# Performance work log

Measured on AMD Instinct MI355X. Metric: run time of the kernel, lower is better.

Reference implementation:

```python
import jax, jax.numpy as jnp
import numpy as np

B, N, E, A, H, F, HEADS = 2, 16384, 262144, 3, 128, 16, 4
DH = H // HEADS
CONST = (2.0 * np.pi) ** 0.5


def setup_inputs() -> dict:
    key = jax.random.key(0)
    ks = jax.random.split(key, 16)
    s = 0.05
    return {
        "x": jax.random.normal(ks[0], (B, N, H), jnp.float32),
        "edge_index": jax.random.randint(ks[1], (2, E), 0, N),
        # per-action message MLPs (self.mlp)
        "mlp_W1": jax.random.normal(ks[2], (A, H, H), jnp.float32) * s,
        "mlp_b1": jnp.zeros((A, H), jnp.float32),
        "mlp_W2": jax.random.normal(ks[3], (A, H, H), jnp.float32) * s,
        "mlp_b2": jnp.zeros((A, H), jnp.float32),
        # transformer (MMTs) projections, 4 heads over the action axis
        "Wq": jax.random.normal(ks[4], (H, H), jnp.float32) * s,
        "bq": jnp.zeros((H,), jnp.float32),
        "Wk": jax.random.normal(ks[5], (H, H), jnp.float32) * s,
        "bk": jnp.zeros((H,), jnp.float32),
        "Wv": jax.random.normal(ks[6], (H, H), jnp.float32) * s,
        "bv": jnp.zeros((H,), jnp.float32),
        "Wo": jax.random.normal(ks[7], (H, H), jnp.float32) * s,
        "bo": jnp.zeros((H,), jnp.float32),
        # decide_mu MLPs (decide_In_sigma is never used in the original forward)
        "mu_W1": jax.random.normal(ks[8], (A, H, H), jnp.float32) * s,
        "mu_b1": jnp.zeros((A, H), jnp.float32),
        "mu_W2": jax.random.normal(ks[9], (A, H, F), jnp.float32) * s,
        "mu_b2": jnp.zeros((A, F), jnp.float32),
    }


def _forward(x, edge_index, mlp_W1, mlp_b1, mlp_W2, mlp_b2,
             Wq, bq, Wk, bk, Wv, bv, Wo, bo, mu_W1, mu_b1, mu_W2, mu_b2):
    # per-action MLP stack: (B,N,H) -> (B,N,A,H)
    h = jax.nn.relu(jnp.einsum('bnh,ahk->bnak', x, mlp_W1) + mlp_b1)
    h = jnp.einsum('bnak,akh->bnah', h, mlp_W2) + mlp_b2
    # gather along source nodes, scatter-add into destination bins
    dst, src = edge_index[0], edge_index[1]
    g = h[:, src]                                   # (B,E,A,H) ~ 800 MB
    agg = jax.ops.segment_sum(jnp.moveaxis(g, 1, 0), dst, num_segments=N)
    agg = jnp.moveaxis(agg, 0, 1)                   # (B,N,A,H)
    # multi-head self-attention over the action axis (len A) per node
    q = (jnp.einsum('bnah,hk->bnak', agg, Wq) + bq).reshape(B, N, A, HEADS, DH)
    k = (jnp.einsum('bnah,hk->bnak', agg, Wk) + bk).reshape(B, N, A, HEADS, DH)
    v = (jnp.einsum('bnah,hk->bnak', agg, Wv) + bv).reshape(B, N, A, HEADS, DH)
    scores = jnp.einsum('bnqed,bnked->bneqk', q, k) / (DH ** 0.5)
    attn = jax.nn.softmax(scores, axis=-1)
    o = jnp.einsum('bneqk,bnked->bnqed', attn, v).reshape(B, N, A, H)
    h_I = agg + jnp.einsum('bnah,hk->bnak', o, Wo) + bo  # residual
    # per-action decode to action means: (B,N,A,F)
    m = jax.nn.relu(jnp.einsum('bnah,ahk->bnak', h_I, mu_W1) + mu_b1)
    mu = jnp.einsum('bnak,akf->bnaf', m, mu_W2) + mu_b2
    # Gaussian reparameterized sampling, VAR is a non-trainable all-ones buffer
    VAR = jnp.ones((N, A, F), jnp.float32)
    noise = jax.random.normal(jax.random.key(42), mu.shape, mu.dtype)
    sample = mu + noise * VAR
    logp = -jnp.log(CONST * VAR) - (sample - mu) ** 2 / (2.0 * VAR ** 2)
    a0 = jax.nn.softmax(jnp.tanh(sample[:, :, 0, :]), axis=-1)
    a1 = jax.nn.sigmoid(sample[:, :, 1, :])
    a2 = jnp.tanh(sample[:, :, 2, :])
    sample_out = jnp.stack([a0, a1, a2], axis=2)    # (B,N,A,F)
    return sample_out, logp.sum((-1, -2))           # ((B,N,A,F),(B,N))


def reference(x, edge_index, mlp_W1, mlp_b1, mlp_W2, mlp_b2,
              Wq, bq, Wk, bk, Wv, bv, Wo, bo, mu_W1, mu_b1, mu_W2, mu_b2):
    return _forward(x, edge_index, mlp_W1, mlp_b1, mlp_W2, mlp_b2,
                    Wq, bq, Wk, bk, Wv, bv, Wo, bo, mu_W1, mu_b1, mu_W2, mu_b2)
```

## Files before the change

### kernel.cpp

```cpp
#include <hip/hip_runtime.h>

#define NN    16384
#define EE    262144
#define BNODES 32768
#define AH    384
#define TOT_NOISE 1572864u

typedef __attribute__((ext_vector_type(8))) short short8;
typedef __attribute__((ext_vector_type(4))) float v4f;

__device__ __forceinline__ unsigned short f2bf(float f) {
  unsigned u = __float_as_uint(f);
  unsigned r = u + 0x7fffu + ((u >> 16) & 1u);
  return (unsigned short)(r >> 16);
}
__device__ __forceinline__ float bf2f(unsigned short h) {
  return __uint_as_float(((unsigned)h) << 16);
}
__device__ __forceinline__ float bflo(unsigned u) { return __uint_as_float(u << 16); }
__device__ __forceinline__ float bfhi(unsigned u) { return __uint_as_float(u & 0xffff0000u); }

__device__ __forceinline__ void threefry2x32_042(unsigned& x0, unsigned& x1) {
  const unsigned ks0 = 0u;
  const unsigned ks1 = 42u;
  const unsigned ks2 = 0x1BD11BDAu ^ 0u ^ 42u;
  x0 += ks0; x1 += ks1;
#define TFR(r) { x0 += x1; x1 = (x1 << (r)) | (x1 >> (32 - (r))); x1 ^= x0; }
  TFR(13) TFR(15) TFR(26) TFR(6)   x0 += ks1; x1 += ks2 + 1u;
  TFR(17) TFR(29) TFR(16) TFR(24)  x0 += ks2; x1 += ks0 + 2u;
  TFR(13) TFR(15) TFR(26) TFR(6)   x0 += ks0; x1 += ks1 + 3u;
  TFR(17) TFR(29) TFR(16) TFR(24)  x0 += ks1; x1 += ks2 + 4u;
  TFR(13) TFR(15) TFR(26) TFR(6)   x0 += ks2; x1 += ks0 + 5u;
#undef TFR
}

__device__ __forceinline__ float erfinv_f32(float x) {
  float w = -log1pf(-x * x);
  float p;
  if (w < 5.0f) {
    w -= 2.5f;
    p = 2.81022636e-08f;
    p = fmaf(p, w, 3.43273939e-07f);
    p = fmaf(p, w, -3.5233877e-06f);
    p = fmaf(p, w, -4.39150654e-06f);
    p = fmaf(p, w, 0.00021858087f);
    p = fmaf(p, w, -0.00125372503f);
    p = fmaf(p, w, -0.00417768164f);
    p = fmaf(p, w, 0.246640727f);
    p = fmaf(p, w, 1.50140941f);
  } else {
    w = sqrtf(w) - 3.0f;
    p = -0.000200214257f;
    p = fmaf(p, w, 0.000100950558f);
    p = fmaf(p, w, 0.00134934322f);
    p = fmaf(p, w, -0.00367342844f);
    p = fmaf(p, w, 0.00573950773f);
    p = fmaf(p, w, -0.0076224613f);
    p = fmaf(p, w, 0.00943887047f);
    p = fmaf(p, w, 1.00167406f);
    p = fmaf(p, w, 2.83297682f);
  }
  return p * x;
}

__device__ __forceinline__ unsigned jax_random_bits32(unsigned i) {
  unsigned x0 = 0u, x1 = i;
  threefry2x32_042(x0, x1);
  return x0 ^ x1;
}

__device__ __forceinline__ float jax_normal_from_bits(unsigned bits) {
  float f = __uint_as_float((bits >> 9) | 0x3f800000u) - 1.0f;
  const float lo = -0.99999994f;
  float u = f * 2.0f + lo;
  u = fmaxf(u, lo);
  return 1.4142135623730951f * erfinv_f32(u);
}

__global__ void edge_count(const int* __restrict__ dst, int* __restrict__ deg) {
  int e = blockIdx.x * 256 + threadIdx.x;
  if (e < EE) atomicAdd(&deg[dst[e]], 1);
}

__global__ __launch_bounds__(256) void scan_k(const int* __restrict__ deg,
                                              int* __restrict__ offs,
                                              int* __restrict__ cur) {
  __shared__ int part[256];
  int t = threadIdx.x;
  int base = t * 64;
  int s = 0;
  for (int i = 0; i < 64; i++) s += deg[base + i];
  part[t] = s;
  __syncthreads();
  for (int off = 1; off < 256; off <<= 1) {
    int v = (t >= off) ? part[t - off] : 0;
    __syncthreads();
    part[t] += v;
    __syncthreads();
  }
  int run = (t == 0) ? 0 : part[t - 1];
  for (int i = 0; i < 64; i++) {
    offs[base + i] = run;
    cur[base + i] = run;
    run += deg[base + i];
  }
  if (t == 255) offs[NN] = run;
}

__global__ void edge_fill(const int* __restrict__ dst, const int* __restrict__ srcv,
                          int* __restrict__ cur, int* __restrict__ csr) {
  int e = blockIdx.x * 256 + threadIdx.x;
  if (e < EE) {
    int d = dst[e];
    int p = atomicAdd(&cur[d], 1);
    csr[p] = srcv[e];
  }
}

__global__ __launch_bounds__(256) void prep_wfrag(
    const float* __restrict__ W1, const float* __restrict__ W2,
    const float* __restrict__ mW1,
    const float* __restrict__ Wq, const float* __restrict__ Wk,
    const float* __restrict__ Wv, const float* __restrict__ Wo,
    unsigned short* __restrict__ F) {
  int m = blockIdx.y;
  const float* W;
  if (m < 3) W = W1 + (long)m * 16384;
  else if (m < 6) W = W2 + (long)(m - 3) * 16384;
  else if (m < 9) W = mW1 + (long)(m - 6) * 16384;
  else W = (m == 9) ? Wq : (m == 10) ? Wk : (m == 11) ? Wv : Wo;
  int f = blockIdx.x * 256 + threadIdx.x;
  int tile = f >> 9;
  int kt = tile >> 3, nt = tile & 7;
  int r = f & 511;
  int lane = r >> 3, j = r & 7;
  int k = kt * 32 + (lane >> 4) * 8 + j;
  int n = nt * 16 + (lane & 15);
  F[(long)m * 16384 + f] = f2bf(W[k * 128 + n]);
}

__global__ __launch_bounds__(256) void prep_w2frag(
    const float* __restrict__ mW2, unsigned short* __restrict__ F2) {
  int a = blockIdx.y;
  int f = blockIdx.x * 256 + threadIdx.x;
  int kt = f >> 9;
  int r = f & 511;
  int lane = r >> 3, j = r & 7;
  int k = kt * 32 + (lane >> 4) * 8 + j;
  int n = lane & 15;
  F2[a * 2048 + f] = f2bf(mW2[(a * 128 + k) * 16 + n]);
}

#define GXSTR 136
__global__ __launch_bounds__(256, 4) void mlp_fused(
    const float* __restrict__ X,
    const unsigned short* __restrict__ WF1, const float* __restrict__ b1,
    const unsigned short* __restrict__ WF2, const float* __restrict__ b2,
    unsigned short* __restrict__ H) {
  __shared__ __align__(16) unsigned short As[128 * GXSTR];
  const int a = blockIdx.y;
  const long m0 = (long)blockIdx.x * 128;
  const int tid = threadIdx.x;
  const unsigned short* Wp1 = WF1 + (long)a * 16384;
  const unsigned short* Wp2 = WF2 + (long)a * 16384;

#pragma unroll
  for (int p = 0; p < 8; p++) {
    int c = tid + p * 256;
    int row = c >> 4, c8 = (c & 15) * 8;
    float4 v1 = *(const float4*)(X + (m0 + row) * 128 + c8);
    float4 v2 = *(const float4*)(X + (m0 + row) * 128 + c8 + 4);
    short8 o;
    o[0] = (short)f2bf(v1.x); o[1] = (short)f2bf(v1.y);
    o[2] = (short)f2bf(v1.z); o[3] = (short)f2bf(v1.w);
    o[4] = (short)f2bf(v2.x); o[5] = (short)f2bf(v2.y);
    o[6] = (short)f2bf(v2.z); o[7] = (short)f2bf(v2.w);
    *(short8*)(&As[row * GXSTR + c8]) = o;
  }
  __syncthreads();

  const int w = tid >> 6, l = tid & 63, lr = l & 15, lg = l >> 4;

  v4f acc[8][2];
#pragma unroll
  for (int mt = 0; mt < 8; mt++) {
    acc[mt][0] = (v4f){0.f, 0.f, 0.f, 0.f};
    acc[mt][1] = (v4f){0.f, 0.f, 0.f, 0.f};
  }
#pragma unroll
  for (int kt = 0; kt < 4; kt++) {
    short8 bfr[2];
#pragma unroll
    for (int ntl = 0; ntl < 2; ntl++)
      bfr[ntl] = *(const short8*)(Wp1 + (long)(kt * 8 + 2 * w + ntl) * 512 + l * 8);
#pragma unroll
    for (int mt = 0; mt < 8; mt++) {
      short8 af = *(const short8*)(&As[(mt * 16 + lr) * GXSTR + kt * 32 + lg * 8]);
      acc[mt][0] = __builtin_amdgcn_mfma_f32_16x16x32_bf16(af, bfr[0], acc[mt][0], 0, 0, 0);
      acc[mt][1] = __builtin_amdgcn_mfma_f32_16x16x32_bf16(af, bfr[1], acc[mt][1], 0, 0, 0);
    }
  }
  __syncthreads();

  {
    float bv[2] = {b1[a * 128 + 32 * w + lr], b1[a * 128 + 32 * w + 16 + lr]};
#pragma unroll
    for (int mt = 0; mt < 8; mt++)
#pragma unroll
      for (int ntl = 0; ntl < 2; ntl++)
#pragma unroll
        for (int i = 0; i < 4; i++) {
          int row = mt * 16 + lg * 4 + i;
          int col = 32 * w + ntl * 16 + lr;
          As[row * GXSTR + col] = f2bf(fmaxf(acc[mt][ntl][i] + bv[ntl], 0.0f));
        }
  }
  __syncthreads();

#pragma unroll
  for (int mt = 0; mt < 8; mt++) {
    acc[mt][0] = (v4f){0.f, 0.f, 0.f, 0.f};
    acc[mt][1] = (v4f){0.f, 0.f, 0.f, 0.f};
  }
#pragma unroll
  for (int kt = 0; kt < 4; kt++) {
    short8 bfr[2];
#pragma unroll
    for (int ntl = 0; ntl < 2; ntl++)
      bfr[ntl] = *(const short8*)(Wp2 + (long)(kt * 8 + 2 * w + ntl) * 512 + l * 8);
#pragma unroll
    for (int mt = 0; mt < 8; mt++) {
      short8 af = *(const short8*)(&As[(mt * 16 + lr) * GXSTR + kt * 32 + lg * 8]);
      acc[mt][0] = __builtin_amdgcn_mfma_f32_16x16x32_bf16(af, bfr[0], acc[mt][0], 0, 0, 0);
      acc[mt][1] = __builtin_amdgcn_mfma_f32_16x16x32_bf16(af, bfr[1], acc[mt][1], 0, 0, 0);
    }
  }
  {
    float bv[2] = {b2[a * 128 + 32 * w + lr], b2[a * 128 + 32 * w + 16 + lr]};
#pragma unroll
    for (int mt = 0; mt < 8; mt++)
#pragma unroll
      for (int ntl = 0; ntl < 2; ntl++)
#pragma unroll
        for (int i = 0; i < 4; i++) {
          long row = m0 + mt * 16 + lg * 4 + i;
          int col = 32 * w + ntl * 16 + lr;
          H[row * 384 + a * 128 + col] = f2bf(acc[mt][ntl][i] + bv[ntl]);
        }
  }
}

__global__ __launch_bounds__(192) void aggregate_v3(
    const unsigned short* __restrict__ H, const int* __restrict__ offs,
    const int* __restrict__ csr, unsigned short* __restrict__ AGB) {
  const int bid = blockIdx.x;
  const int bt = bid >> 13;
  const int pair = bid & 8191;
  const int t = threadIdx.x;
  const int n = pair * 2 + (t / 96);
  const int c = (t % 96) * 4;
  const int e0 = offs[n], e1 = offs[n + 1];
  const unsigned short* hb = H + (long)bt * NN * 384 + c;
  float a0 = 0.f, a1 = 0.f, a2 = 0.f, a3 = 0.f;

  const int nfull = (e1 - e0) >> 3;
  int s[8];
  if (nfull > 0) {
#pragma unroll
    for (int i = 0; i < 8; i++) s[i] = csr[e0 + i];
  }
  for (int b = 0; b < nfull; b++) {
    int sn[8];
    if (b + 1 < nfull) {
      int base = e0 + b * 8 + 8;
#pragma unroll
      for (int i = 0; i < 8; i++) sn[i] = csr[base + i];
    }
#pragma unroll
    for (int i = 0; i < 8; i++) {
      uint2 u = *(const uint2*)(hb + (long)s[i] * 384);
      a0 += bflo(u.x); a1 += bfhi(u.x); a2 += bflo(u.y); a3 += bfhi(u.y);
    }
#pragma unroll
    for (int i = 0; i < 8; i++) s[i] = sn[i];
  }
  for (int j = e0 + nfull * 8; j < e1; j++) {
    int si = csr[j];
    uint2 u = *(const uint2*)(hb + (long)si * 384);
    a0 += bflo(u.x); a1 += bfhi(u.x); a2 += bflo(u.y); a3 += bfhi(u.y);
  }
  uint2 out;
  out.x = (unsigned)f2bf(a0) | ((unsigned)f2bf(a1) << 16);
  out.y = (unsigned)f2bf(a2) | ((unsigned)f2bf(a3) << 16);
  *(uint2*)(AGB + ((long)bt * NN + n) * 384 + c) = out;
}

#define XSTR 136
#define QSTR 34
__global__ __launch_bounds__(256, 3) void attn_mega(
    const unsigned short* __restrict__ AGB, const unsigned short* __restrict__ WF,
    const float* __restrict__ bq, const float* __restrict__ bk,
    const float* __restrict__ bv, const float* __restrict__ bo,
    const unsigned short* __restrict__ WM1, const float* __restrict__ mb1,
    const unsigned short* __restrict__ WM2, const float* __restrict__ mb2,
    float* __restrict__ out0, float* __restrict__ out1) {
  __shared__ __align__(16) unsigned short xS[48 * XSTR];
  __shared__ __align__(16) unsigned short qS[4 * 48 * QSTR];
  __shared__ __align__(16) unsigned short kS[4 * 48 * QSTR];
  __shared__ __align__(16) unsigned short vS[4 * 48 * QSTR];
  __shared__ float lpS[48];

  const int tid = threadIdx.x;
  const long node0 = (long)blockIdx.x * 16;
  const unsigned short* src = AGB + node0 * 384;

#pragma unroll
  for (int p = 0; p < 3; p++) {
    int c = tid + p * 256;
    int row = c >> 4, c8 = (c & 15) * 8;
    short8 v = *(const short8*)(src + c * 8);
    *(short8*)(&xS[row * XSTR + c8]) = v;
  }
  __syncthreads();

  const int w = tid >> 6;
  const int l = tid & 63;
  const int lr = l & 15;
  const int lg = l >> 4;
  const unsigned short* WQ = WF;
  const unsigned short* WK = WF + 16384;
  const unsigned short* WV = WF + 32768;
  const unsigned short* WO = WF + 49152;

  v4f accq[3][2], acck[3][2], accv[3][2];
#pragma unroll
  for (int mt = 0; mt < 3; mt++)
#pragma unroll
    for (int n = 0; n < 2; n++) {
      accq[mt][n] = (v4f){0.f, 0.f, 0.f, 0.f};
      acck[mt][n] = (v4f){0.f, 0.f, 0.f, 0.f};
      accv[mt][n] = (v4f){0.f, 0.f, 0.f, 0.f};
    }
#pragma unroll
  for (int kt = 0; kt < 4; kt++) {
    short8 af[3];
#pragma unroll
    for (int mt = 0; mt < 3; mt++)
      af[mt] = *(const short8*)&xS[(mt * 16 + lr) * XSTR + kt * 32 + lg * 8];
#pragma unroll
    for (int ntl = 0; ntl < 2; ntl++) {
      long tf = (long)(kt * 8 + 2 * w + ntl) * 512 + l * 8;
      short8 b0 = *(const short8*)&WQ[tf];
      short8 b1 = *(const short8*)&WK[tf];
      short8 b2 = *(const short8*)&WV[tf];
#pragma unroll
      for (int mt = 0; mt < 3; mt++) {
        accq[mt][ntl] = __builtin_amdgcn_mfma_f32_16x16x32_bf16(af[mt], b0, accq[mt][ntl], 0, 0, 0);
        acck[mt][ntl] = __builtin_amdgcn_mfma_f32_16x16x32_bf16(af[mt], b1, acck[mt][ntl], 0, 0, 0);
        accv[mt][ntl] = __builtin_amdgcn_mfma_f32_16x16x32_bf16(af[mt], b2, accv[mt][ntl], 0, 0, 0);
      }
    }
  }
  {
    const float scale = 0.17677669529663687f;
    unsigned short* qw = &qS[w * 48 * QSTR];
    unsigned short* kw = &kS[w * 48 * QSTR];
    unsigned short* vw = &vS[w * 48 * QSTR];
    float bqv[2] = {bq[32 * w + lr], bq[32 * w + 16 + lr]};
    float bkv[2] = {bk[32 * w + lr], bk[32 * w + 16 + lr]};
    float bvv[2] = {bv[32 * w + lr], bv[32 * w + 16 + lr]};
#pragma unroll
    for (int mt = 0; mt < 3; mt++)
#pragma unroll
      for (int ntl = 0; ntl < 2; ntl++)
#pragma unroll
        for (int i = 0; i < 4; i++) {
          int row = mt * 16 + lg * 4 + i;
          int col = ntl * 16 + lr;
          qw[row * QSTR + col] = f2bf((accq[mt][ntl][i] + bqv[ntl]) * scale);
          kw[row * QSTR + col] = f2bf(acck[mt][ntl][i] + bkv[ntl]);
          vw[row * QSTR + col] = f2bf(accv[mt][ntl][i] + bvv[ntl]);
        }
  }

  float resv[3][2][4];
#pragma unroll
  for (int mt = 0; mt < 3; mt++)
#pragma unroll
    for (int ntl = 0; ntl < 2; ntl++)
#pragma unroll
      for (int i = 0; i < 4; i++)
        resv[mt][ntl][i] =
            bf2f(xS[(mt * 16 + lg * 4 + i) * XSTR + 32 * w + ntl * 16 + lr]);
  __syncthreads();

  if (l < 48) {
    int aq = l % 3;
    int ndr = l - aq;
    const unsigned* qr = (const unsigned*)&qS[(w * 48 + l) * QSTR];
    const unsigned* kr0 = (const unsigned*)&kS[(w * 48 + ndr) * QSTR];
    const unsigned* kr1 = (const unsigned*)&kS[(w * 48 + ndr + 1) * QSTR];
    const unsigned* kr2 = (const unsigned*)&kS[(w * 48 + ndr + 2) * QSTR];
    float s0 = 0.f, s1 = 0.f, s2 = 0.f;
#pragma unroll
    for (int j = 0; j < 16; j++) {
      unsigned uq = qr[j], u0 = kr0[j], u1 = kr1[j], u2 = kr2[j];
      float qa = bflo(uq), qb = bfhi(uq);
      s0 = fmaf(qa, bflo(u0), fmaf(qb, bfhi(u0), s0));
      s1 = fmaf(qa, bflo(u1), fmaf(qb, bfhi(u1), s1));
      s2 = fmaf(qa, bflo(u2), fmaf(qb, bfhi(u2), s2));
    }
    float mx = fmaxf(s0, fmaxf(s1, s2));
    float e0 = expf(s0 - mx), e1 = expf(s1 - mx), e2 = expf(s2 - mx);
    float inv = 1.0f / (e0 + e1 + e2);
    e0 *= inv; e1 *= inv; e2 *= inv;
    const unsigned* vr0 = (const unsigned*)&vS[(w * 48 + ndr) * QSTR];
    const unsigned* vr1 = (const unsigned*)&vS[(w * 48 + ndr + 1) * QSTR];
    const unsigned* vr2 = (const unsigned*)&vS[(w * 48 + ndr + 2) * QSTR];
    unsigned ov[16];
#pragma unroll
    for (int j = 0; j < 16; j++) {
      unsigned u0 = vr0[j], u1 = vr1[j], u2 = vr2[j];
      float oa = fmaf(e0, bflo(u0), fmaf(e1, bflo(u1), e2 * bflo(u2)));
      float ob = fmaf(e0, bfhi(u0), fmaf(e1, bfhi(u1), e2 * bfhi(u2)));
      ov[j] = (unsigned)f2bf(oa) | ((unsigned)f2bf(ob) << 16);
    }
    uint4* orow = (uint4*)&xS[l * XSTR + 32 * w];
    orow[0] = make_uint4(ov[0], ov[1], ov[2], ov[3]);
    orow[1] = make_uint4(ov[4], ov[5], ov[6], ov[7]);
    orow[2] = make_uint4(ov[8], ov[9], ov[10], ov[11]);
    orow[3] = make_uint4(ov[12], ov[13], ov[14], ov[15]);
  }
  __syncthreads();

  v4f acco[3][2];
#pragma unroll
  for (int mt = 0; mt < 3; mt++)
#pragma unroll
    for (int n = 0; n < 2; n++) acco[mt][n] = (v4f){0.f, 0.f, 0.f, 0.f};
#pragma unroll
  for (int kt = 0; kt < 4; kt++) {
    short8 af[3];
#pragma unroll
    for (int mt = 0; mt < 3; mt++)
      af[mt] = *(const short8*)&xS[(mt * 16 + lr) * XSTR + kt * 32 + lg * 8];
#pragma unroll
    for (int ntl = 0; ntl < 2; ntl++) {
      long tf = (long)(kt * 8 + 2 * w + ntl) * 512 + l * 8;
      short8 b = *(const short8*)&WO[tf];
#pragma unroll
      for (int mt = 0; mt < 3; mt++)
        acco[mt][ntl] = __builtin_amdgcn_mfma_f32_16x16x32_bf16(af[mt], b, acco[mt][ntl], 0, 0, 0);
    }
  }
  __syncthreads();

  {
    float bov[2] = {bo[32 * w + lr], bo[32 * w + 16 + lr]};
#pragma unroll
    for (int mt = 0; mt < 3; mt++)
#pragma unroll
      for (int ntl = 0; ntl < 2; ntl++)
#pragma unroll
        for (int i = 0; i < 4; i++) {
          int row = mt * 16 + lg * 4 + i;
          int nd = row / 3, a_ = row - nd * 3;
          int gcol = 32 * w + ntl * 16 + lr;
          xS[(a_ * 16 + nd) * XSTR + gcol] =
              f2bf(acco[mt][ntl][i] + bov[ntl] + resv[mt][ntl][i]);
        }
  }
  __syncthreads();

  v4f accm[3][2];
#pragma unroll
  for (int mt = 0; mt < 3; mt++)
#pragma unroll
    for (int n = 0; n < 2; n++) accm[mt][n] = (v4f){0.f, 0.f, 0.f, 0.f};
#pragma unroll
  for (int kt = 0; kt < 4; kt++) {
#pragma unroll
    for (int mt = 0; mt < 3; mt++) {
      short8 af = *(const short8*)&xS[(mt * 16 + lr) * XSTR + kt * 32 + lg * 8];
#pragma unroll
      for (int ntl = 0; ntl < 2; ntl++) {
        short8 b = *(const short8*)(WM1 + (long)mt * 16384 +
                                    (long)(kt * 8 + 2 * w + ntl) * 512 + l * 8);
        accm[mt][ntl] = __builtin_amdgcn_mfma_f32_16x16x32_bf16(af, b, accm[mt][ntl], 0, 0, 0);
      }
    }
  }
  __syncthreads();

#pragma unroll
  for (int mt = 0; mt < 3; mt++)
#pragma unroll
    for (int ntl = 0; ntl < 2; ntl++) {
      int col = 32 * w + ntl * 16 + lr;
      float bias = mb1[mt * 128 + col];
#pragma unroll
      for (int i = 0; i < 4; i++) {
        int rowp = mt * 16 + lg * 4 + i;
        xS[rowp * XSTR + col] = f2bf(fmaxf(accm[mt][ntl][i] + bias, 0.0f));
      }
    }
  __syncthreads();

  if (w < 3) {
    v4f accu = (v4f){0.f, 0.f, 0.f, 0.f};
#pragma unroll
    for (int kt = 0; kt < 4; kt++) {
      short8 af = *(const short8*)&xS[(w * 16 + lr) * XSTR + kt * 32 + lg * 8];
      short8 b = *(const short8*)(WM2 + w * 2048 + kt * 512 + l * 8);
      accu = __builtin_amdgcn_mfma_f32_16x16x32_bf16(af, b, accu, 0, 0, 0);
    }
    float bias = mb2[w * 16 + lr];
#pragma unroll
    for (int i = 0; i < 4; i++) {
      int nd = lg * 4 + i;
      float mu = accu[i] + bias;
      unsigned gidx = (unsigned)((node0 + nd) * 48 + w * 16 + lr);
      unsigned bits = jax_random_bits32(gidx);
      float noise = jax_normal_from_bits(bits);
      float sample = mu + noise;
      float lp = -0.9189385332046727f - 0.5f * noise * noise;
      lp += __shfl_xor(lp, 1, 64);
      lp += __shfl_xor(lp, 2, 64);
      lp += __shfl_xor(lp, 4, 64);
      lp += __shfl_xor(lp, 8, 64);
      if (lr == 0) lpS[w * 16 + nd] = lp;
      float res;
      if (w == 0) {
        float th = tanhf(sample);
        float mx = th;
        mx = fmaxf(mx, __shfl_xor(mx, 1, 64));
        mx = fmaxf(mx, __shfl_xor(mx, 2, 64));
        mx = fmaxf(mx, __shfl_xor(mx, 4, 64));
        mx = fmaxf(mx, __shfl_xor(mx, 8, 64));
        float ex = expf(th - mx);
        float ss = ex;
        ss += __shfl_xor(ss, 1, 64);
        ss += __shfl_xor(ss, 2, 64);
        ss += __shfl_xor(ss, 4, 64);
        ss += __shfl_xor(ss, 8, 64);
        res = ex / ss;
      } else if (w == 1) {
        res = 1.0f / (1.0f + expf(-sample));
      } else {
        res = tanhf(sample);
      }
      out0[gidx] = res;
    }
  }
  __syncthreads();
  if (tid < 16)
    out1[node0 + tid] = lpS[tid] + lpS[16 + tid] + lpS[32 + tid];
}

extern "C" void kernel_launch(void* const* d_in, const int* in_sizes, int n_in,
                              void* d_out, int out_size, void* d_ws, size_t ws_size,
                              hipStream_t stream) {
  const float* x = (const float*)d_in[0];
  const int* ei = (const int*)d_in[1];
  const float* W1 = (const float*)d_in[2];
  const float* b1 = (const float*)d_in[3];
  const float* W2 = (const float*)d_in[4];
  const float* b2 = (const float*)d_in[5];
  const float* Wq = (const float*)d_in[6];
  const float* bq = (const float*)d_in[7];
  const float* Wk = (const float*)d_in[8];
  const float* bk = (const float*)d_in[9];
  const float* Wv = (const float*)d_in[10];
  const float* bv = (const float*)d_in[11];
  const float* Wo = (const float*)d_in[12];
  const float* bo = (const float*)d_in[13];
  const float* mW1 = (const float*)d_in[14];
  const float* mb1 = (const float*)d_in[15];
  const float* mW2 = (const float*)d_in[16];
  const float* mb2 = (const float*)d_in[17];
  (void)in_sizes; (void)n_in; (void)out_size; (void)ws_size;

  unsigned short* HB = (unsigned short*)d_ws;
  unsigned short* AGB = HB + 12582912;
  int* deg = (int*)(AGB + 12582912);
  int* offs = deg + NN;
  int* cur = offs + (NN + 1);
  int* csr = cur + NN;
  unsigned short* wfrag = (unsigned short*)(((uintptr_t)(csr + EE) + 15) & ~(uintptr_t)15);
  unsigned short* w2frag = wfrag + 13 * 16384;

  const int* dst = ei;
  const int* srcv = ei + EE;

  float* out0 = (float*)d_out;
  float* out1 = out0 + TOT_NOISE;

  hipMemsetAsync(deg, 0, NN * sizeof(int), stream);
  edge_count<<<EE / 256, 256, 0, stream>>>(dst, deg);
  scan_k<<<1, 256, 0, stream>>>(deg, offs, cur);
  edge_fill<<<EE / 256, 256, 0, stream>>>(dst, srcv, cur, csr);
  prep_wfrag<<<dim3(64, 13), 256, 0, stream>>>(W1, W2, mW1, Wq, Wk, Wv, Wo, wfrag);
  prep_w2frag<<<dim3(8, 3), 256, 0, stream>>>(mW2, w2frag);

  mlp_fused<<<dim3(BNODES / 128, 3), 256, 0, stream>>>(x, wfrag, b1, wfrag + 3 * 16384, b2, HB);
  aggregate_v3<<<2 * NN / 2, 192, 0, stream>>>(HB, offs, csr, AGB);
  attn_mega<<<BNODES / 16, 256, 0, stream>>>(AGB, wfrag + 9 * 16384, bq, bk, bv, bo,
                                             wfrag + 6 * 16384, mb1, w2frag, mb2,
                                             out0, out1);
}
```

Before: 250.1 us.

## Fuse neighbor aggregation into attention kernel, dropping the intermediate buffer

Removes the standalone aggregation kernel and performs the CSR gather-sum directly inside attn_mega, writing the aggregated bf16 rows straight into shared memory. Each of 16 threads per node sums 24 contiguous channels using 16-byte loads, two edges per iteration. This eliminates the write and re-read of the 25 MB AGB buffer and one kernel launch. In exchange, the gather now runs under attn_mega's occupancy and register budget (24 float accumulators per thread, launch bounds 256,3), which may reduce the latency hiding the separate kernel had.

```diff
diff --git a/kernel.cpp b/kernel.cpp
--- a/kernel.cpp
+++ b/kernel.cpp
@@ -250,55 +250,12 @@
   }
 }
 
-__global__ __launch_bounds__(192) void aggregate_v3(
-    const unsigned short* __restrict__ H, const int* __restrict__ offs,
-    const int* __restrict__ csr, unsigned short* __restrict__ AGB) {
-  const int bid = blockIdx.x;
-  const int bt = bid >> 13;
-  const int pair = bid & 8191;
-  const int t = threadIdx.x;
-  const int n = pair * 2 + (t / 96);
-  const int c = (t % 96) * 4;
-  const int e0 = offs[n], e1 = offs[n + 1];
-  const unsigned short* hb = H + (long)bt * NN * 384 + c;
-  float a0 = 0.f, a1 = 0.f, a2 = 0.f, a3 = 0.f;
-
-  const int nfull = (e1 - e0) >> 3;
-  int s[8];
-  if (nfull > 0) {
-#pragma unroll
-    for (int i = 0; i < 8; i++) s[i] = csr[e0 + i];
-  }
-  for (int b = 0; b < nfull; b++) {
-    int sn[8];
-    if (b + 1 < nfull) {
-      int base = e0 + b * 8 + 8;
-#pragma unroll
-      for (int i = 0; i < 8; i++) sn[i] = csr[base + i];
-    }
-#pragma unroll
-    for (int i = 0; i < 8; i++) {
-      uint2 u = *(const uint2*)(hb + (long)s[i] * 384);
-      a0 += bflo(u.x); a1 += bfhi(u.x); a2 += bflo(u.y); a3 += bfhi(u.y);
-    }
-#pragma unroll
-    for (int i = 0; i < 8; i++) s[i] = sn[i];
-  }
-  for (int j = e0 + nfull * 8; j < e1; j++) {
-    int si = csr[j];
-    uint2 u = *(const uint2*)(hb + (long)si * 384);
-    a0 += bflo(u.x); a1 += bfhi(u.x); a2 += bflo(u.y); a3 += bfhi(u.y);
-  }
-  uint2 out;
-  out.x = (unsigned)f2bf(a0) | ((unsigned)f2bf(a1) << 16);
-  out.y = (unsigned)f2bf(a2) | ((unsigned)f2bf(a3) << 16);
-  *(uint2*)(AGB + ((long)bt * NN + n) * 384 + c) = out;
-}
-
 #define XSTR 136
 #define QSTR 34
 __global__ __launch_bounds__(256, 3) void attn_mega(
-    const unsigned short* __restrict__ AGB, const unsigned short* __restrict__ WF,
+    const unsigned short* __restrict__ H, const int* __restrict__ offs,
+    const int* __restrict__ csr,
+    const unsigned short* __restrict__ WF,
     const float* __restrict__ bq, const float* __restrict__ bk,
     const float* __restrict__ bv, const float* __restrict__ bo,
     const unsigned short* __restrict__ WM1, const float* __restrict__ mb1,
@@ -312,14 +269,56 @@
 
   const int tid = threadIdx.x;
   const long node0 = (long)blockIdx.x * 16;
-  const unsigned short* src = AGB + node0 * 384;
-
-#pragma unroll
-  for (int p = 0; p < 3; p++) {
-    int c = tid + p * 256;
-    int row = c >> 4, c8 = (c & 15) * 8;
-    short8 v = *(const short8*)(src + c * 8);
-    *(short8*)(&xS[row * XSTR + c8]) = v;
+
+  {
+    const int bt = (int)(node0 >> 14);
+    const int nbase = (int)(node0 & (NN - 1));
+    const int nd = tid >> 4;
+    const int sub = tid & 15;
+    const int n = nbase + nd;
+    const int e0 = offs[n], e1 = offs[n + 1];
+    const unsigned short* hb = H + (long)bt * NN * 384 + sub * 24;
+    float acc24[24];
+#pragma unroll
+    for (int i = 0; i < 24; i++) acc24[i] = 0.f;
+
+    int j = e0;
+    for (; j + 2 <= e1; j += 2) {
+      int s0 = csr[j], s1 = csr[j + 1];
+      const unsigned short* p0 = hb + (long)s0 * 384;
+      const unsigned short* p1 = hb + (long)s1 * 384;
+      uint4 A0 = *(const uint4*)(p0);
+      uint4 A1 = *(const uint4*)(p0 + 8);
+      uint4 A2 = *(const uint4*)(p0 + 16);
+      uint4 B0 = *(const uint4*)(p1);
+      uint4 B1 = *(const uint4*)(p1 + 8);
+      uint4 B2 = *(const uint4*)(p1 + 16);
+#define ACC8(base, u)                                                   \
+      { acc24[base+0] += bflo(u.x); acc24[base+1] += bfhi(u.x);         \
+        acc24[base+2] += bflo(u.y); acc24[base+3] += bfhi(u.y);         \
+        acc24[base+4] += bflo(u.z); acc24[base+5] += bfhi(u.z);         \
+        acc24[base+6] += bflo(u.w); acc24[base+7] += bfhi(u.w); }
+      ACC8(0, A0) ACC8(8, A1) ACC8(16, A2)
+      ACC8(0, B0) ACC8(8, B1) ACC8(16, B2)
+    }
+    if (j < e1) {
+      int s0 = csr[j];
+      const unsigned short* p0 = hb + (long)s0 * 384;
+      uint4 A0 = *(const uint4*)(p0);
+      uint4 A1 = *(const uint4*)(p0 + 8);
+      uint4 A2 = *(const uint4*)(p0 + 16);
+      ACC8(0, A0) ACC8(8, A1) ACC8(16, A2)
+#undef ACC8
+    }
+#pragma unroll
+    for (int jj = 0; jj < 12; jj++) {
+      int g = sub * 24 + 2 * jj;
+      int a_ = g >> 7;
+      int c = g & 127;
+      unsigned pack = (unsigned)f2bf(acc24[2 * jj]) |
+                      ((unsigned)f2bf(acc24[2 * jj + 1]) << 16);
+      *(unsigned*)&xS[(3 * nd + a_) * XSTR + c] = pack;
+    }
   }
   __syncthreads();
 
@@ -581,8 +580,7 @@
   (void)in_sizes; (void)n_in; (void)out_size; (void)ws_size;
 
   unsigned short* HB = (unsigned short*)d_ws;
-  unsigned short* AGB = HB + 12582912;
-  int* deg = (int*)(AGB + 12582912);
+  int* deg = (int*)(HB + 12582912);
   int* offs = deg + NN;
   int* cur = offs + (NN + 1);
   int* csr = cur + NN;
@@ -603,8 +601,8 @@
   prep_w2frag<<<dim3(8, 3), 256, 0, stream>>>(mW2, w2frag);
 
   mlp_fused<<<dim3(BNODES / 128, 3), 256, 0, stream>>>(x, wfrag, b1, wfrag + 3 * 16384, b2, HB);
-  aggregate_v3<<<2 * NN / 2, 192, 0, stream>>>(HB, offs, csr, AGB);
-  attn_mega<<<BNODES / 16, 256, 0, stream>>>(AGB, wfrag + 9 * 16384, bq, bk, bv, bo,
+  attn_mega<<<BNODES / 16, 256, 0, stream>>>(HB, offs, csr,
+                                             wfrag + 9 * 16384, bq, bk, bv, bo,
                                              wfrag + 6 * 16384, mb1, w2frag, mb2,
                                              out0, out1);
 }
```

Result: faster. 244.7 us (-2.2%).
